# Optimization experiments

Measured on AMD Instinct MI355X. Metric: run time of the kernel, lower is better.

Reference implementation:

```python
import jax, jax.numpy as jnp
import numpy as np

NUM_VERTEX = 1448
C = 256


def _decode(latent, eye_labels, left_mu, left_delta, right_mu, right_delta):
    # latent: [B, C, H, W] -> global average pool -> [B, C]
    lat = jnp.mean(latent, axis=(-2, -1))
    # batched decode against both eye models, select per-sample by eye label
    left = lat @ left_delta.T + left_mu[:, 0]    # [B, 3*N]
    right = lat @ right_delta.T + right_mu[:, 0]  # [B, 3*N]
    pts = jnp.where(eye_labels[:, None] == 1, right, left)
    return pts.reshape(lat.shape[0], NUM_VERTEX, 3)  # [B, N, 3]


def _cdist(a, b):
    # Euclidean distance via the norm trick; a,b: [B, N, 3]
    a2 = jnp.sum(a * a, axis=-1)  # [B, N]
    b2 = jnp.sum(b * b, axis=-1)  # [B, M]
    d2 = a2[:, :, None] + b2[:, None, :] - 2.0 * jnp.einsum('bnd,bmd->bnm', a, b)
    return jnp.sqrt(jnp.maximum(d2, 1e-12))


def setup_inputs() -> dict:
    key = jax.random.key(0)
    ks = jax.random.split(key, 8)
    B, H, W = 64, 8, 8
    inputs = jax.random.normal(ks[0], (B, C, H, W), dtype=jnp.float32)
    targets = jax.random.normal(ks[1], (B, C, H, W), dtype=jnp.float32)
    eye_labels = jax.random.randint(ks[2], (B,), 0, 2)
    left_mu = jax.random.normal(ks[3], (3 * NUM_VERTEX, 1), dtype=jnp.float32)
    left_delta = jax.random.normal(ks[4], (3 * NUM_VERTEX, C), dtype=jnp.float32) * 0.1
    right_mu = jax.random.normal(ks[5], (3 * NUM_VERTEX, 1), dtype=jnp.float32)
    right_delta = jax.random.normal(ks[6], (3 * NUM_VERTEX, C), dtype=jnp.float32) * 0.1
    return {"inputs": inputs, "targets": targets, "eye_labels": eye_labels,
            "left_mu": left_mu, "left_delta": left_delta,
            "right_mu": right_mu, "right_delta": right_delta}


def reference(inputs, targets, eye_labels, left_mu, left_delta, right_mu, right_delta):
    pts_in = _decode(inputs, eye_labels, left_mu, left_delta, right_mu, right_delta)
    pts_tg = _decode(targets, eye_labels, left_mu, left_delta, right_mu, right_delta)
    d = _cdist(pts_in, pts_tg)  # [B, N, N]
    dist_1 = jnp.mean(jnp.min(d, axis=-1))
    dist_2 = jnp.mean(jnp.min(d, axis=-2))
    return dist_1 + dist_2
```

## Files before the change

kernel.cpp:

```cpp
#include <hip/hip_runtime.h>

#define NV 1448
#define JD 4344
#define CC 256
#define BB 64
#define QQ 128
#define NPAD32 1472
#define NTR 46
#define NRSL 8
#define PADV 60000.0f

typedef __bf16    bf16x8 __attribute__((ext_vector_type(8)));
typedef _Float16  f16x8  __attribute__((ext_vector_type(8)));
typedef float     f32x4  __attribute__((ext_vector_type(4)));
typedef float     f32x16 __attribute__((ext_vector_type(16)));

__device__ __forceinline__ unsigned f2bf(float f) {
    unsigned u = __float_as_uint(f);
    return (u + 0x7FFFu + ((u >> 16) & 1u)) >> 16;
}
union HU { _Float16 h; unsigned short u; };
__device__ __forceinline__ unsigned short f2h(float f) { HU t; t.h = (_Float16)f; return t.u; }
__device__ __forceinline__ float h2f(unsigned short u) { HU t; t.u = u; return (float)t.h; }

#define MIN3(dst, a, b, c) asm("v_min3_f32 %0, %1, %2, %3" : "=v"(dst) : "v"(a), "v"(b), "v"(c))
#define MIN3A(dst, a, b)   asm("v_min3_f32 %0, %0, %1, %2" : "+v"(dst) : "v"(a), "v"(b))

__global__ __launch_bounds__(256) void pool_kernel(const float* __restrict__ inp,
                                                   const float* __restrict__ tgt,
                                                   unsigned short* __restrict__ latQb,
                                                   unsigned long long* __restrict__ acc) {
    int gid  = blockIdx.x * 256 + threadIdx.x;
    if (gid == 0) { acc[0] = 0ull; acc[1] = 0ull; }
    int lane = gid & 15;
    int row  = gid >> 4;
    if (row >= 2 * BB * CC) return;
    int t  = row >> 14;
    int bc = row & 16383;
    const float* src = (t ? tgt : inp) + (size_t)bc * 64;
    float4 v = reinterpret_cast<const float4*>(src)[lane];
    float s = (v.x + v.y) + (v.z + v.w);
    s += __shfl_xor(s, 1);
    s += __shfl_xor(s, 2);
    s += __shfl_xor(s, 4);
    s += __shfl_xor(s, 8);
    if (lane == 0) {
        int b = bc >> 8, c = bc & 255;
        latQb[(size_t)(t * 64 + b) * CC + c] = (unsigned short)f2bf(s * (1.0f / 64.0f));
    }
}

__global__ __launch_bounds__(256) void decode_kernel(const unsigned short* __restrict__ latQb,
                                                     const float* __restrict__ muL,
                                                     const float* __restrict__ deltaL,
                                                     const float* __restrict__ muR,
                                                     const float* __restrict__ deltaR,
                                                     const int* __restrict__ labels,
                                                     float* __restrict__ pts3) {
    const int jt   = blockIdx.x;
    const int side = blockIdx.y;
    const int qq   = blockIdx.z;
    const float* __restrict__ delta = side ? deltaR : deltaL;
    const float* __restrict__ mu    = side ? muR : muL;
    const int jb = jt * 64;
    const int q0 = qq * 32;
    const int tid  = threadIdx.x;
    const int w    = tid >> 6;
    const int lane = tid & 63;

    __shared__ unsigned short dB[64 * 264];
    __shared__ unsigned short lB[32 * 264];

#pragma unroll
    for (int i = 0; i < 16; ++i) {
        int idx = i * 256 + tid;
        int row = idx >> 6;
        int ch  = idx & 63;
        int j   = jb + row;
        unsigned u0 = 0, u1 = 0;
        if (j < JD) {
            float4 v = *reinterpret_cast<const float4*>(delta + (size_t)j * CC + ch * 4);
            u0 = f2bf(v.x) | (f2bf(v.y) << 16);
            u1 = f2bf(v.z) | (f2bf(v.w) << 16);
        }
        *reinterpret_cast<uint2*>(&dB[row * 264 + ch * 4]) = make_uint2(u0, u1);
    }
#pragma unroll
    for (int i = 0; i < 4; ++i) {
        int idx = i * 256 + tid;
        int row = idx >> 5;
        int ch  = idx & 31;
        *reinterpret_cast<uint4*>(&lB[row * 264 + ch * 8]) =
            *reinterpret_cast<const uint4*>(latQb + (size_t)(q0 + row) * CC + ch * 8);
    }
    __syncthreads();

    const int col  = lane & 15;
    const int kgrp = lane >> 4;
    bf16x8 bfr[8];
#pragma unroll
    for (int ks = 0; ks < 8; ++ks)
        bfr[ks] = *reinterpret_cast<const bf16x8*>(&dB[(w * 16 + col) * 264 + ks * 32 + kgrp * 8]);

    int j = jb + w * 16 + col;
    float muv = (j < JD) ? mu[j] : 0.f;

#pragma unroll
    for (int mt = 0; mt < 2; ++mt) {
        f32x4 acc = {0.f, 0.f, 0.f, 0.f};
#pragma unroll
        for (int ks = 0; ks < 8; ++ks) {
            bf16x8 a = *reinterpret_cast<const bf16x8*>(&lB[(mt * 16 + col) * 264 + ks * 32 + kgrp * 8]);
            acc = __builtin_amdgcn_mfma_f32_16x16x32_bf16(a, bfr[ks], acc, 0, 0, 0);
        }
        if (j < JD) {
#pragma unroll
            for (int r = 0; r < 4; ++r) {
                int q = q0 + mt * 16 + kgrp * 4 + r;
                if (labels[q & 63] == side)
                    pts3[(size_t)q * JD + j] = acc[r] + muv;
            }
        }
    }
}

__global__ __launch_bounds__(256) void pack_kernel(const float* __restrict__ pts3,
                                                   unsigned short* __restrict__ Apack,
                                                   unsigned short* __restrict__ Bpack) {
    int idx = blockIdx.x * 256 + threadIdx.x;
    if (idx >= QQ * NPAD32) return;
    int q = idx / NPAD32;
    int n = idx - q * NPAD32;
    float x = 0.f, y = 0.f, z = 0.f;
    bool real = n < NV;
    if (real) {
        const float* p = pts3 + (size_t)q * JD + n * 3;
        x = p[0]; y = p[1]; z = p[2];
    }
    float p2 = fmaf(x, x, fmaf(y, y, z * z));
    if (!real) p2 = PADV;
    unsigned short p2h = f2h(p2);
    unsigned short p2l = f2h(p2 - h2f(p2h));
    unsigned short one = f2h(1.0f);
    unsigned short out[16];
    if (q < BB) {
        unsigned short ahx = f2h(-2.f * x), ahy = f2h(-2.f * y), ahz = f2h(-2.f * z);
        unsigned short alx = f2h(-2.f * x - h2f(ahx));
        unsigned short aly = f2h(-2.f * y - h2f(ahy));
        unsigned short alz = f2h(-2.f * z - h2f(ahz));
        out[0] = ahx; out[1] = ahx; out[2] = alx;
        out[3] = ahy; out[4] = ahy; out[5] = aly;
        out[6] = ahz; out[7] = ahz; out[8] = alz;
        out[9] = one; out[10] = one; out[11] = p2h; out[12] = p2l;
        out[13] = out[14] = out[15] = 0;
        uint4* dst = reinterpret_cast<uint4*>(Apack + ((size_t)q * NPAD32 + n) * 16);
        dst[0] = *reinterpret_cast<uint4*>(&out[0]);
        dst[1] = *reinterpret_cast<uint4*>(&out[8]);
    } else {
        unsigned short bhx = f2h(x), bhy = f2h(y), bhz = f2h(z);
        unsigned short blx = f2h(x - h2f(bhx));
        unsigned short bly = f2h(y - h2f(bhy));
        unsigned short blz = f2h(z - h2f(bhz));
        out[0] = bhx; out[1] = blx; out[2] = bhx;
        out[3] = bhy; out[4] = bly; out[5] = bhy;
        out[6] = bhz; out[7] = blz; out[8] = bhz;
        out[9] = p2h; out[10] = p2l; out[11] = one; out[12] = one;
        out[13] = out[14] = out[15] = 0;
        uint4* dst = reinterpret_cast<uint4*>(Bpack + ((size_t)(q - BB) * NPAD32 + n) * 16);
        dst[0] = *reinterpret_cast<uint4*>(&out[0]);
        dst[1] = *reinterpret_cast<uint4*>(&out[8]);
    }
}

__global__ __launch_bounds__(256) void chamfer_kernel(const unsigned short* __restrict__ Apack,
                                                      const unsigned short* __restrict__ Bpack,
                                                      float* __restrict__ cmin,
                                                      unsigned long long* __restrict__ acc) {
    const int b      = blockIdx.x;
    const int rslice = blockIdx.y;
    const int tr0    = rslice * 6;
    const int ntr    = (rslice == 7) ? 4 : 6;
    const int tid  = threadIdx.x;
    const int w    = tid >> 6;
    const int lane = tid & 63;
    const int col  = lane & 31;
    const int half = lane >> 5;

    __shared__ unsigned short BsL[NPAD32 * 16];
    __shared__ float rmw[4][64][17];
    __shared__ float wsum[4];

    {
        const uint4* src = reinterpret_cast<const uint4*>(Bpack + (size_t)b * NPAD32 * 16);
        uint4* dst = reinterpret_cast<uint4*>(BsL);
        for (int i = tid; i < NPAD32 * 2; i += 256)
            dst[i ^ ((i >> 3) & 7)] = src[i];
    }
    __syncthreads();

    const int tcs[5] = {0, 12, 24, 35, 46};
    const int my0 = tcs[w], my1 = tcs[w + 1];
    const int nslots = my1 - my0;

    float cmAcc[12];
#pragma unroll
    for (int i = 0; i < 12; ++i) cmAcc[i] = 1e30f;

    f32x16 zero16;
#pragma unroll
    for (int i = 0; i < 16; ++i) zero16[i] = 0.f;

    float ssum = 0.f;
    const char* Bb = (const char*)BsL;

#define BFRAG(tc) (*reinterpret_cast<const f16x8*>(Bb + 16 * ((((tc) * 64 + col * 2 + half)) ^ (((((tc) * 64 + col * 2 + half)) >> 3) & 7))))
#define CTREE(dd, slot) do { float t0, t1, t2v, t3, t4, u0, u1; \
    MIN3(t0, dd[0], dd[1], dd[2]);   MIN3(t1, dd[3], dd[4], dd[5]); \
    MIN3(t2v, dd[6], dd[7], dd[8]);  MIN3(t3, dd[9], dd[10], dd[11]); \
    MIN3(t4, dd[12], dd[13], dd[14]); \
    MIN3(u0, t0, t1, t2v); MIN3(u1, t3, t4, dd[15]); \
    MIN3A(cmAcc[slot], u0, u1); } while (0)

    for (int trl = 0; trl < ntr; ++trl) {
        const int tr = tr0 + trl;
        f16x8 afr = *reinterpret_cast<const f16x8*>(
            Apack + ((size_t)b * NPAD32 + tr * 32 + col) * 16 + half * 8);

        float rm[16];
#pragma unroll
        for (int i = 0; i < 16; ++i) rm[i] = 1e30f;

        int t2 = my0;
        for (; t2 + 1 < my1; t2 += 2) {
            f16x8 bf0 = BFRAG(t2);
            f16x8 bf1 = BFRAG(t2 + 1);
            f32x16 d0 = __builtin_amdgcn_mfma_f32_32x32x16_f16(afr, bf0, zero16, 0, 0, 0);
            f32x16 d1 = __builtin_amdgcn_mfma_f32_32x32x16_f16(afr, bf1, zero16, 0, 0, 0);
#pragma unroll
            for (int i = 0; i < 16; ++i)
                MIN3A(rm[i], d0[i], d1[i]);
            CTREE(d0, t2 - my0);
            CTREE(d1, t2 + 1 - my0);
        }
        if (t2 < my1) {
            f16x8 bf0 = BFRAG(t2);
            f32x16 d0 = __builtin_amdgcn_mfma_f32_32x32x16_f16(afr, bf0, zero16, 0, 0, 0);
#pragma unroll
            for (int i = 0; i < 16; ++i) rm[i] = fminf(rm[i], d0[i]);
            CTREE(d0, t2 - my0);
        }

#pragma unroll
        for (int i = 0; i < 16; ++i) rmw[w][lane][i] = rm[i];
        __syncthreads();
        {
            int R = tid >> 3, k = tid & 7;
            int reg = (R & 3) | ((R >> 3) << 2);
            int h   = (R >> 2) & 1;
            float v = 1e30f;
#pragma unroll
            for (int ww = 0; ww < 4; ++ww) {
                v = fminf(v, rmw[ww][h * 32 + k][reg]);
                v = fminf(v, rmw[ww][h * 32 + k + 8][reg]);
                v = fminf(v, rmw[ww][h * 32 + k + 16][reg]);
                v = fminf(v, rmw[ww][h * 32 + k + 24][reg]);
            }
            v = fminf(v, __shfl_xor(v, 1));
            v = fminf(v, __shfl_xor(v, 2));
            v = fminf(v, __shfl_xor(v, 4));
            if (k == 0) {
                int row = tr * 32 + R;
                if (row < NV) ssum += sqrtf(fmaxf(v, 1e-12f));
            }
        }
        __syncthreads();
    }

#pragma unroll
    for (int s = 0; s < 12; ++s) {
        if (s < nslots) {
            float cmv = fminf(cmAcc[s], __shfl_xor(cmAcc[s], 32));
            if (half == 0) {
                int tc = my0 + s;
                cmin[((size_t)rslice * BB + b) * NPAD32 + tc * 32 + col] = cmv;
            }
        }
    }

    ssum += __shfl_xor(ssum, 1);
    ssum += __shfl_xor(ssum, 2);
    ssum += __shfl_xor(ssum, 4);
    ssum += __shfl_xor(ssum, 8);
    ssum += __shfl_xor(ssum, 16);
    ssum += __shfl_xor(ssum, 32);
    if ((tid & 63) == 0) wsum[w] = ssum;
    __syncthreads();
    if (tid == 0) {
        float bs = (wsum[0] + wsum[1]) + (wsum[2] + wsum[3]);
        atomicAdd(acc, (unsigned long long)((double)bs * 16777216.0));
    }
}

__global__ __launch_bounds__(256) void combine_kernel(const float* __restrict__ cmin,
                                                      unsigned long long* __restrict__ acc,
                                                      float* __restrict__ out) {
    int idx = blockIdx.x * 256 + threadIdx.x;
    int b = idx / NPAD32;
    int n = idx - b * NPAD32;
    float s = 0.f;
    if (n < NV) {
        float v = 1e30f;
#pragma unroll
        for (int sl = 0; sl < NRSL; ++sl)
            v = fminf(v, cmin[((size_t)sl * BB + b) * NPAD32 + n]);
        s = sqrtf(fmaxf(v, 1e-12f));
    }
    s += __shfl_xor(s, 1);
    s += __shfl_xor(s, 2);
    s += __shfl_xor(s, 4);
    s += __shfl_xor(s, 8);
    s += __shfl_xor(s, 16);
    s += __shfl_xor(s, 32);
    __shared__ float wsum[4];
    if ((threadIdx.x & 63) == 0) wsum[threadIdx.x >> 6] = s;
    __syncthreads();
    if (threadIdx.x == 0) {
        float bs = (wsum[0] + wsum[1]) + (wsum[2] + wsum[3]);
        atomicAdd(acc, (unsigned long long)((double)bs * 16777216.0));
        __threadfence();
        unsigned long long done = atomicAdd(acc + 1, 1ull);
        if (done == 367) {
            __threadfence();
            unsigned long long total = atomicAdd(acc, 0ull);
            out[0] = (float)((double)total * (0x1p-24 / (64.0 * 1448.0)));
        }
    }
}

extern "C" void kernel_launch(void* const* d_in, const int* in_sizes, int n_in,
                              void* d_out, int out_size, void* d_ws, size_t ws_size,
                              hipStream_t stream) {
    const float* inp    = (const float*)d_in[0];
    const float* tgt    = (const float*)d_in[1];
    const int*   labels = (const int*)d_in[2];
    const float* muL    = (const float*)d_in[3];
    const float* deltaL = (const float*)d_in[4];
    const float* muR    = (const float*)d_in[5];
    const float* deltaR = (const float*)d_in[6];
    float* out = (float*)d_out;

    char* ws = (char*)d_ws;
    unsigned short* latQb = (unsigned short*)ws;
    float* pts3           = (float*)(ws + 65536);
    unsigned short* Apack = (unsigned short*)(ws + 2289664);
    unsigned short* Bpack = (unsigned short*)(ws + 5304320);
    float* cmin           = (float*)(ws + 8318976);
    unsigned long long* acc = (unsigned long long*)(ws + 11333632);

    hipLaunchKernelGGL(pool_kernel, dim3(2048), dim3(256), 0, stream, inp, tgt, latQb, acc);
    hipLaunchKernelGGL(decode_kernel, dim3(68, 2, 4), dim3(256), 0, stream,
                       latQb, muL, deltaL, muR, deltaR, labels, pts3);
    hipLaunchKernelGGL(pack_kernel, dim3(736), dim3(256), 0, stream, pts3, Apack, Bpack);
    hipLaunchKernelGGL(chamfer_kernel, dim3(BB, NRSL), dim3(256), 0, stream,
                       Apack, Bpack, cmin, acc);
    hipLaunchKernelGGL(combine_kernel, dim3(368), dim3(256), 0, stream, cmin, acc, out);
}
```

Before: 60.52 us.

## Compute both chamfer directions as row-min passes and drop the combine kernel

Instead of deriving column minima through a per-column min tree, cmin writes and a separate combine kernel, the pack kernel now emits both A and B packings for every point set. The chamfer kernel launches twice as many blocks, one per direction, each doing only row minima. This removes the column-min reduction, the cmin buffer traffic and one kernel launch. In exchange the number of MFMA distance tiles doubles and the pack kernel writes twice as much data. The final reduction moves into the chamfer kernel via a block counter.

```diff
diff --git a/kernel.cpp b/kernel.cpp
--- a/kernel.cpp
+++ b/kernel.cpp
@@ -5,9 +5,7 @@
 #define CC 256
 #define BB 64
 #define QQ 128
-#define NPAD32 1472
-#define NTR 46
-#define NRSL 8
+#define NP 1472
 #define PADV 60000.0f
 
 typedef __bf16    bf16x8 __attribute__((ext_vector_type(8)));
@@ -23,8 +21,7 @@
 __device__ __forceinline__ unsigned short f2h(float f) { HU t; t.h = (_Float16)f; return t.u; }
 __device__ __forceinline__ float h2f(unsigned short u) { HU t; t.u = u; return (float)t.h; }
 
-#define MIN3(dst, a, b, c) asm("v_min3_f32 %0, %1, %2, %3" : "=v"(dst) : "v"(a), "v"(b), "v"(c))
-#define MIN3A(dst, a, b)   asm("v_min3_f32 %0, %0, %1, %2" : "+v"(dst) : "v"(a), "v"(b))
+#define MIN3A(dst, a, b) asm("v_min3_f32 %0, %0, %1, %2" : "+v"(dst) : "v"(a), "v"(b))
 
 __global__ __launch_bounds__(256) void pool_kernel(const float* __restrict__ inp,
                                                    const float* __restrict__ tgt,
@@ -125,12 +122,12 @@
 }
 
 __global__ __launch_bounds__(256) void pack_kernel(const float* __restrict__ pts3,
-                                                   unsigned short* __restrict__ Apack,
-                                                   unsigned short* __restrict__ Bpack) {
+                                                   unsigned short* __restrict__ packA,
+                                                   unsigned short* __restrict__ packB) {
     int idx = blockIdx.x * 256 + threadIdx.x;
-    if (idx >= QQ * NPAD32) return;
-    int q = idx / NPAD32;
-    int n = idx - q * NPAD32;
+    if (idx >= QQ * NP) return;
+    int q = idx / NP;
+    int n = idx - q * NP;
     float x = 0.f, y = 0.f, z = 0.f;
     bool real = n < NV;
     if (real) {
@@ -142,69 +139,57 @@
     unsigned short p2h = f2h(p2);
     unsigned short p2l = f2h(p2 - h2f(p2h));
     unsigned short one = f2h(1.0f);
-    unsigned short out[16];
-    if (q < BB) {
-        unsigned short ahx = f2h(-2.f * x), ahy = f2h(-2.f * y), ahz = f2h(-2.f * z);
-        unsigned short alx = f2h(-2.f * x - h2f(ahx));
-        unsigned short aly = f2h(-2.f * y - h2f(ahy));
-        unsigned short alz = f2h(-2.f * z - h2f(ahz));
-        out[0] = ahx; out[1] = ahx; out[2] = alx;
-        out[3] = ahy; out[4] = ahy; out[5] = aly;
-        out[6] = ahz; out[7] = ahz; out[8] = alz;
-        out[9] = one; out[10] = one; out[11] = p2h; out[12] = p2l;
-        out[13] = out[14] = out[15] = 0;
-        uint4* dst = reinterpret_cast<uint4*>(Apack + ((size_t)q * NPAD32 + n) * 16);
-        dst[0] = *reinterpret_cast<uint4*>(&out[0]);
-        dst[1] = *reinterpret_cast<uint4*>(&out[8]);
-    } else {
-        unsigned short bhx = f2h(x), bhy = f2h(y), bhz = f2h(z);
-        unsigned short blx = f2h(x - h2f(bhx));
-        unsigned short bly = f2h(y - h2f(bhy));
-        unsigned short blz = f2h(z - h2f(bhz));
-        out[0] = bhx; out[1] = blx; out[2] = bhx;
-        out[3] = bhy; out[4] = bly; out[5] = bhy;
-        out[6] = bhz; out[7] = blz; out[8] = bhz;
-        out[9] = p2h; out[10] = p2l; out[11] = one; out[12] = one;
-        out[13] = out[14] = out[15] = 0;
-        uint4* dst = reinterpret_cast<uint4*>(Bpack + ((size_t)(q - BB) * NPAD32 + n) * 16);
-        dst[0] = *reinterpret_cast<uint4*>(&out[0]);
-        dst[1] = *reinterpret_cast<uint4*>(&out[8]);
-    }
-}
-
-__global__ __launch_bounds__(256) void chamfer_kernel(const unsigned short* __restrict__ Apack,
-                                                      const unsigned short* __restrict__ Bpack,
-                                                      float* __restrict__ cmin,
-                                                      unsigned long long* __restrict__ acc) {
+
+    unsigned short ahx = f2h(-2.f * x), ahy = f2h(-2.f * y), ahz = f2h(-2.f * z);
+    unsigned short alx = f2h(-2.f * x - h2f(ahx));
+    unsigned short aly = f2h(-2.f * y - h2f(ahy));
+    unsigned short alz = f2h(-2.f * z - h2f(ahz));
+    unsigned short outA[16] = {ahx, ahx, alx, ahy, ahy, aly, ahz, ahz, alz,
+                               one, one, p2h, p2l, 0, 0, 0};
+    uint4* dA = reinterpret_cast<uint4*>(packA + ((size_t)q * NP + n) * 16);
+    dA[0] = *reinterpret_cast<uint4*>(&outA[0]);
+    dA[1] = *reinterpret_cast<uint4*>(&outA[8]);
+
+    unsigned short bhx = f2h(x), bhy = f2h(y), bhz = f2h(z);
+    unsigned short blx = f2h(x - h2f(bhx));
+    unsigned short bly = f2h(y - h2f(bhy));
+    unsigned short blz = f2h(z - h2f(bhz));
+    unsigned short outB[16] = {bhx, blx, bhx, bhy, bly, bhy, bhz, blz, bhz,
+                               p2h, p2l, one, one, 0, 0, 0};
+    uint4* dB = reinterpret_cast<uint4*>(packB + ((size_t)(q ^ 64) * NP + n) * 16);
+    dB[0] = *reinterpret_cast<uint4*>(&outB[0]);
+    dB[1] = *reinterpret_cast<uint4*>(&outB[8]);
+}
+
+__global__ __launch_bounds__(256) void chamfer_kernel(const unsigned short* __restrict__ packA,
+                                                      const unsigned short* __restrict__ packB,
+                                                      unsigned long long* __restrict__ acc,
+                                                      float* __restrict__ out) {
     const int b      = blockIdx.x;
-    const int rslice = blockIdx.y;
-    const int tr0    = rslice * 6;
+    const int dir    = blockIdx.y;
+    const int rslice = blockIdx.z;
     const int ntr    = (rslice == 7) ? 4 : 6;
     const int tid  = threadIdx.x;
     const int w    = tid >> 6;
     const int lane = tid & 63;
     const int col  = lane & 31;
     const int half = lane >> 5;
-
-    __shared__ unsigned short BsL[NPAD32 * 16];
+    const size_t pb = (size_t)(dir * BB + b) * NP;
+
+    __shared__ unsigned short BsL[NP * 16];
     __shared__ float rmw[4][64][17];
     __shared__ float wsum[4];
 
     {
-        const uint4* src = reinterpret_cast<const uint4*>(Bpack + (size_t)b * NPAD32 * 16);
+        const uint4* src = reinterpret_cast<const uint4*>(packB + pb * 16);
         uint4* dst = reinterpret_cast<uint4*>(BsL);
-        for (int i = tid; i < NPAD32 * 2; i += 256)
+        for (int i = tid; i < NP * 2; i += 256)
             dst[i ^ ((i >> 3) & 7)] = src[i];
     }
     __syncthreads();
 
-    const int tcs[5] = {0, 12, 24, 35, 46};
-    const int my0 = tcs[w], my1 = tcs[w + 1];
-    const int nslots = my1 - my0;
-
-    float cmAcc[12];
-#pragma unroll
-    for (int i = 0; i < 12; ++i) cmAcc[i] = 1e30f;
+    const int tc0 = (w * 46) >> 2;
+    const int tc1 = ((w + 1) * 46) >> 2;
 
     f32x16 zero16;
 #pragma unroll
@@ -212,42 +197,37 @@
 
     float ssum = 0.f;
     const char* Bb = (const char*)BsL;
-
-#define BFRAG(tc) (*reinterpret_cast<const f16x8*>(Bb + 16 * ((((tc) * 64 + col * 2 + half)) ^ (((((tc) * 64 + col * 2 + half)) >> 3) & 7))))
-#define CTREE(dd, slot) do { float t0, t1, t2v, t3, t4, u0, u1; \
-    MIN3(t0, dd[0], dd[1], dd[2]);   MIN3(t1, dd[3], dd[4], dd[5]); \
-    MIN3(t2v, dd[6], dd[7], dd[8]);  MIN3(t3, dd[9], dd[10], dd[11]); \
-    MIN3(t4, dd[12], dd[13], dd[14]); \
-    MIN3(u0, t0, t1, t2v); MIN3(u1, t3, t4, dd[15]); \
-    MIN3A(cmAcc[slot], u0, u1); } while (0)
+    const char* Ab = (const char*)packA;
 
     for (int trl = 0; trl < ntr; ++trl) {
-        const int tr = tr0 + trl;
+        const int tr = rslice * 6 + trl;
         f16x8 afr = *reinterpret_cast<const f16x8*>(
-            Apack + ((size_t)b * NPAD32 + tr * 32 + col) * 16 + half * 8);
+            Ab + (pb + (size_t)(tr * 32 + col)) * 32 + half * 16);
 
         float rm[16];
 #pragma unroll
         for (int i = 0; i < 16; ++i) rm[i] = 1e30f;
 
-        int t2 = my0;
-        for (; t2 + 1 < my1; t2 += 2) {
-            f16x8 bf0 = BFRAG(t2);
-            f16x8 bf1 = BFRAG(t2 + 1);
-            f32x16 d0 = __builtin_amdgcn_mfma_f32_32x32x16_f16(afr, bf0, zero16, 0, 0, 0);
-            f32x16 d1 = __builtin_amdgcn_mfma_f32_32x32x16_f16(afr, bf1, zero16, 0, 0, 0);
-#pragma unroll
-            for (int i = 0; i < 16; ++i)
-                MIN3A(rm[i], d0[i], d1[i]);
-            CTREE(d0, t2 - my0);
-            CTREE(d1, t2 + 1 - my0);
-        }
-        if (t2 < my1) {
-            f16x8 bf0 = BFRAG(t2);
-            f32x16 d0 = __builtin_amdgcn_mfma_f32_32x32x16_f16(afr, bf0, zero16, 0, 0, 0);
-#pragma unroll
-            for (int i = 0; i < 16; ++i) rm[i] = fminf(rm[i], d0[i]);
-            CTREE(d0, t2 - my0);
+#pragma unroll
+        for (int p = 0; p < 6; ++p) {
+            int tc = tc0 + 2 * p;
+            if (tc + 1 < tc1) {
+                int t0i = tc * 64 + col * 2 + half;
+                int t1i = t0i + 64;
+                f16x8 bf0 = *reinterpret_cast<const f16x8*>(Bb + 16 * (t0i ^ ((t0i >> 3) & 7)));
+                f16x8 bf1 = *reinterpret_cast<const f16x8*>(Bb + 16 * (t1i ^ ((t1i >> 3) & 7)));
+                f32x16 d0 = __builtin_amdgcn_mfma_f32_32x32x16_f16(afr, bf0, zero16, 0, 0, 0);
+                f32x16 d1 = __builtin_amdgcn_mfma_f32_32x32x16_f16(afr, bf1, zero16, 0, 0, 0);
+#pragma unroll
+                for (int i = 0; i < 16; ++i)
+                    MIN3A(rm[i], d0[i], d1[i]);
+            } else if (tc < tc1) {
+                int t0i = tc * 64 + col * 2 + half;
+                f16x8 bf0 = *reinterpret_cast<const f16x8*>(Bb + 16 * (t0i ^ ((t0i >> 3) & 7)));
+                f32x16 d0 = __builtin_amdgcn_mfma_f32_32x32x16_f16(afr, bf0, zero16, 0, 0, 0);
+#pragma unroll
+                for (int i = 0; i < 16; ++i) rm[i] = fminf(rm[i], d0[i]);
+            }
         }
 
 #pragma unroll
@@ -276,17 +256,6 @@
         __syncthreads();
     }
 
-#pragma unroll
-    for (int s = 0; s < 12; ++s) {
-        if (s < nslots) {
-            float cmv = fminf(cmAcc[s], __shfl_xor(cmAcc[s], 32));
-            if (half == 0) {
-                int tc = my0 + s;
-                cmin[((size_t)rslice * BB + b) * NPAD32 + tc * 32 + col] = cmv;
-            }
-        }
-    }
-
     ssum += __shfl_xor(ssum, 1);
     ssum += __shfl_xor(ssum, 2);
     ssum += __shfl_xor(ssum, 4);
@@ -298,38 +267,9 @@
     if (tid == 0) {
         float bs = (wsum[0] + wsum[1]) + (wsum[2] + wsum[3]);
         atomicAdd(acc, (unsigned long long)((double)bs * 16777216.0));
-    }
-}
-
-__global__ __launch_bounds__(256) void combine_kernel(const float* __restrict__ cmin,
-                                                      unsigned long long* __restrict__ acc,
-                                                      float* __restrict__ out) {
-    int idx = blockIdx.x * 256 + threadIdx.x;
-    int b = idx / NPAD32;
-    int n = idx - b * NPAD32;
-    float s = 0.f;
-    if (n < NV) {
-        float v = 1e30f;
-#pragma unroll
-        for (int sl = 0; sl < NRSL; ++sl)
-            v = fminf(v, cmin[((size_t)sl * BB + b) * NPAD32 + n]);
-        s = sqrtf(fmaxf(v, 1e-12f));
-    }
-    s += __shfl_xor(s, 1);
-    s += __shfl_xor(s, 2);
-    s += __shfl_xor(s, 4);
-    s += __shfl_xor(s, 8);
-    s += __shfl_xor(s, 16);
-    s += __shfl_xor(s, 32);
-    __shared__ float wsum[4];
-    if ((threadIdx.x & 63) == 0) wsum[threadIdx.x >> 6] = s;
-    __syncthreads();
-    if (threadIdx.x == 0) {
-        float bs = (wsum[0] + wsum[1]) + (wsum[2] + wsum[3]);
-        atomicAdd(acc, (unsigned long long)((double)bs * 16777216.0));
         __threadfence();
         unsigned long long done = atomicAdd(acc + 1, 1ull);
-        if (done == 367) {
+        if (done == 1023) {
             __threadfence();
             unsigned long long total = atomicAdd(acc, 0ull);
             out[0] = (float)((double)total * (0x1p-24 / (64.0 * 1448.0)));
@@ -352,16 +292,14 @@
     char* ws = (char*)d_ws;
     unsigned short* latQb = (unsigned short*)ws;
     float* pts3           = (float*)(ws + 65536);
-    unsigned short* Apack = (unsigned short*)(ws + 2289664);
-    unsigned short* Bpack = (unsigned short*)(ws + 5304320);
-    float* cmin           = (float*)(ws + 8318976);
-    unsigned long long* acc = (unsigned long long*)(ws + 11333632);
+    unsigned short* packA = (unsigned short*)(ws + 2289664);
+    unsigned short* packB = (unsigned short*)(ws + 8318976);
+    unsigned long long* acc = (unsigned long long*)(ws + 14348288);
 
     hipLaunchKernelGGL(pool_kernel, dim3(2048), dim3(256), 0, stream, inp, tgt, latQb, acc);
     hipLaunchKernelGGL(decode_kernel, dim3(68, 2, 4), dim3(256), 0, stream,
                        latQb, muL, deltaL, muR, deltaR, labels, pts3);
-    hipLaunchKernelGGL(pack_kernel, dim3(736), dim3(256), 0, stream, pts3, Apack, Bpack);
-    hipLaunchKernelGGL(chamfer_kernel, dim3(BB, NRSL), dim3(256), 0, stream,
-                       Apack, Bpack, cmin, acc);
-    hipLaunchKernelGGL(combine_kernel, dim3(368), dim3(256), 0, stream, cmin, acc, out);
-}
+    hipLaunchKernelGGL(pack_kernel, dim3(736), dim3(256), 0, stream, pts3, packA, packB);
+    hipLaunchKernelGGL(chamfer_kernel, dim3(BB, 2, 8), dim3(256), 0, stream,
+                       packA, packB, acc, out);
+}
```

Measured after the change: 74.20 us. 22.6% more time.
